# Kernel optimization log

Hardware: AMD Instinct MI355X
Metric: run time of the kernel (lower is better)

## Reference

```python
import jax, jax.numpy as jnp
import numpy as np

N, DF, DR, H, K = 4096, 128, 64, 1024, 10


def _init_linear(key, fan_in, fan_out):
    kw, kb = jax.random.split(key)
    bound = 1.0 / np.sqrt(fan_in)
    W = jax.random.uniform(kw, (fan_in, fan_out), jnp.float32, -bound, bound)
    b = jax.random.uniform(kb, (fan_out,), jnp.float32, -bound, bound)
    return W, b


def setup_inputs() -> dict:
    key = jax.random.key(0)
    ks = jax.random.split(key, 8)
    condition = jax.random.normal(ks[0], (N, DF), jnp.float32)
    tensor = jax.random.normal(ks[1], (N, DR), jnp.float32)
    Win, b_in = _init_linear(ks[2], DF + DR, H)
    W1, b1 = _init_linear(ks[3], H, H)
    W2, b2 = _init_linear(ks[4], H, H)
    W3, b3 = _init_linear(ks[5], H, H)
    Wout, b_out = _init_linear(ks[6], H, DR)
    return {"condition": condition, "tensor": tensor,
            "Win": Win, "b_in": b_in, "W1": W1, "b1": b1,
            "W2": W2, "b2": b2, "W3": W3, "b3": b3,
            "Wout": Wout, "b_out": b_out}


def _mlp(x, Win, b_in, W1, b1, W2, b2, W3, b3, Wout, b_out):
    # FFNN: input layer + 3 hidden layers with Softplus, linear output -> DR
    h = jax.nn.softplus(x @ Win + b_in)
    h = jax.nn.softplus(h @ W1 + b1)
    h = jax.nn.softplus(h @ W2 + b2)
    h = jax.nn.softplus(h @ W3 + b3)
    return h @ Wout + b_out


def reference(condition, tensor, Win, b_in, W1, b1, W2, b2, W3, b3, Wout, b_out):
    # torch.cdist(condition, condition), p=2 -> [N, N]
    sq = jnp.sum(condition * condition, axis=-1)
    d2 = sq[:, None] + sq[None, :] - 2.0 * (condition @ condition.T)
    dist = jnp.sqrt(jnp.maximum(d2, 0.0))
    # torch.topk(dist, 10, dim=1, largest=False) -> k nearest neighbor indices
    _, neighbor_idx = jax.lax.top_k(-dist, K)  # [N, K]
    # gather neighbor groups
    cond_g = condition[neighbor_idx]  # [N, K, DF]
    tens_g = tensor[neighbor_idx]     # [N, K, DR]
    # MongeMapNetwork.pushforward: tensor - MLP(concat(condition, tensor))
    x = jnp.concatenate([cond_g, tens_g], axis=-1)  # [N, K, DF+DR]
    pushed = tens_g - _mlp(x, Win, b_in, W1, b1, W2, b2, W3, b3, Wout, b_out)
    return pushed  # [N, K, DR]
```

## Files before the change

### kernel.cpp

```cpp
#include <hip/hip_runtime.h>
#include <hip/hip_fp16.h>
#include <stdint.h>

typedef unsigned short u16;
typedef unsigned int   u32;
typedef unsigned long long u64;
typedef short v8bf __attribute__((ext_vector_type(8)));
typedef float v4f  __attribute__((ext_vector_type(4)));
typedef u16   v8u  __attribute__((ext_vector_type(8)));

#define NPTS 4096
#define DF   128
#define DR   64
#define HID  1024
#define KNN  10
#define DIN  192
#define NB   512

#define AS1 __attribute__((address_space(1)))
#define AS3 __attribute__((address_space(3)))

__device__ __forceinline__ float bf2f(u16 b){ return __uint_as_float(((unsigned)b)<<16); }
__device__ __forceinline__ u16 f2bf(float f){
  unsigned u = __float_as_uint(f);
  unsigned r = 0x7fffu + ((u>>16)&1u);
  return (u16)((u + r)>>16);
}
__device__ __forceinline__ u16 f2h(float f){
  __half h = __float2half(f);
  return __half_as_ushort(h);
}
__device__ __forceinline__ float softplus_f(float x){
  return x>15.f ? x : __logf(1.f + __expf(x));
}
__device__ __forceinline__ float rdv(const void* p, long j, int fl){
  return fl ? bf2f(((const u16*)p)[j]) : ((const float*)p)[j];
}
__device__ __forceinline__ void gl2lds16(const u16* g, u16* l){
  __builtin_amdgcn_global_load_lds((const AS1 unsigned int*)g, (AS3 unsigned int*)l, 16, 0, 0);
}

constexpr size_t OFF_BAR   = 0;
constexpr size_t OFF_FLAG  = 128;
constexpr size_t OFF_SQ    = 256;
constexpr size_t OFF_NIDX  = OFF_SQ    + 16384;
constexpr size_t OFF_BIAS  = OFF_NIDX  + 163840;
constexpr size_t OFF_CONDF = OFF_BIAS  + 16640;
constexpr size_t OFF_TENSF = OFF_CONDF + 2097152;
constexpr size_t OFF_WTIN  = OFF_TENSF + 1048576;
constexpr size_t OFF_WT1   = OFF_WTIN  + 393216;
constexpr size_t OFF_WT2   = OFF_WT1   + 2097152;
constexpr size_t OFF_WT3   = OFF_WT2   + 2097152;
constexpr size_t OFF_WTO   = OFF_WT3   + 2097152;
constexpr size_t OFF_DIST  = OFF_WTO   + 131072;
constexpr size_t OFF_X     = OFF_DIST  + 33554432;
constexpr size_t OFF_A0    = OFF_X     + 1572864;
constexpr size_t OFF_A1    = OFF_A0    + 8388608;
constexpr size_t OFF_P     = OFF_A1    + 8388608;

__device__ __forceinline__ void gbar(u32* cnt, u32* rel, u32 e){
  __syncthreads();
  if(threadIdx.x == 0){
    __threadfence();
    u32 a = __hip_atomic_fetch_add(cnt, 1u, __ATOMIC_ACQ_REL, __HIP_MEMORY_SCOPE_AGENT);
    if(a == e*NB + (NB-1)){
      __hip_atomic_store(rel, e+1u, __ATOMIC_RELEASE, __HIP_MEMORY_SCOPE_AGENT);
    } else {
      while(__hip_atomic_load(rel, __ATOMIC_ACQUIRE, __HIP_MEMORY_SCOPE_AGENT) <= e)
        __builtin_amdgcn_s_sleep(2);
    }
    __threadfence();
  }
  __syncthreads();
}

__device__ __forceinline__ int detect_fl(const void* cond, u16* SM){
  const u16* c = (const u16*)cond;
  int tid = threadIdx.x, n = 0;
  for(int i=tid; i<8192; i+=256){
    u16 v = c[2*i];
    int e = (v>>7)&0xff;
    n += (e>=96 && e<=158);
  }
  int* cnt = (int*)SM;
  cnt[tid] = n; __syncthreads();
  for(int s=128; s>0; s>>=1){ if(tid<s) cnt[tid]+=cnt[tid+s]; __syncthreads(); }
  int fl = (cnt[0] > 4915) ? 1 : 0;
  __syncthreads();
  return fl;
}

__device__ __forceinline__ void prep_unit(int u, int tid, int fl,
    const void* cond, const void* tens,
    const void* Wi, const void* W1, const void* W2, const void* W3, const void* Wo,
    const void* bi, const void* b1, const void* b2, const void* b3, const void* bo,
    float* condF, float* tensF, float* biasF,
    u16* Oi, u16* O1, u16* O2, u16* O3, u16* Oo,
    float* sq, u16* X, u16* SM){
  if(u < 3089){
    int i = u*256 + tid;
    if(i < 524288){ condF[i] = rdv(cond, i, fl); }
    else if(i < 786432){ tensF[i-524288] = rdv(tens, i-524288, fl); }
    else{
      int j = i - 786432;
      if(j < 1024)      biasF[j] = rdv(bi, j, fl);
      else if(j < 2048) biasF[j] = rdv(b1, j-1024, fl);
      else if(j < 3072) biasF[j] = rdv(b2, j-2048, fl);
      else if(j < 4096) biasF[j] = rdv(b3, j-3072, fl);
      else if(j < 4160) biasF[j] = rdv(bo, j-4096, fl);
    }
  } else if(u < 6417){
    u16 (*tile)[33] = (u16(*)[33])SM;
    int b = u - 3089;
    const void* in; u16* out; int R, C, bx, by;
    if(b < 192)      {              in=Wi; out=Oi; R=192;  C=1024; bx=b&31; by=b>>5; }
    else if(b < 1216){ b -= 192;    in=W1; out=O1; R=1024; C=1024; bx=b&31; by=b>>5; }
    else if(b < 2240){ b -= 1216;   in=W2; out=O2; R=1024; C=1024; bx=b&31; by=b>>5; }
    else if(b < 3264){ b -= 2240;   in=W3; out=O3; R=1024; C=1024; bx=b&31; by=b>>5; }
    else             { b -= 3264;   in=Wo; out=Oo; R=1024; C=64;   bx=b&1;  by=b>>1; }
    int gx = bx*32, gy = by*32;
    int tx = tid&31, ty = tid>>5;
    #pragma unroll
    for(int r=ty; r<32; r+=8){
      size_t idx = (size_t)(gy+r)*C + gx + tx;
      tile[r][tx] = fl ? ((const u16*)in)[idx] : f2bf(((const float*)in)[idx]);
    }
    __syncthreads();
    #pragma unroll
    for(int r=ty; r<32; r+=8) out[(size_t)(gx+r)*R + gy + tx] = tile[tx][r];
  } else if(u < 7441){
    int b = u - 6417;
    int row = b*4 + (tid>>6), lane = tid&63;
    float a = rdv(cond, (long)row*DF + lane, fl);
    float c2 = rdv(cond, (long)row*DF + lane + 64, fl);
    double s = (double)a*a + (double)c2*c2;
    #pragma unroll
    for(int off=32; off>0; off>>=1) s += __shfl_down(s, off, 64);
    if(lane==0) sq[row] = (float)s;
  } else {
    int c = (u-7441)*256 + tid;
    int j = c/48;
    int off = (c - j*48)*4;
    ushort4 o;
    if(off < DF){
      o.x = f2bf(rdv(cond, (long)j*DF + off + 0, fl));
      o.y = f2bf(rdv(cond, (long)j*DF + off + 1, fl));
      o.z = f2bf(rdv(cond, (long)j*DF + off + 2, fl));
      o.w = f2bf(rdv(cond, (long)j*DF + off + 3, fl));
    }else{
      int t2 = off - DF;
      o.x = f2bf(rdv(tens, (long)j*DR + t2 + 0, fl));
      o.y = f2bf(rdv(tens, (long)j*DR + t2 + 1, fl));
      o.z = f2bf(rdv(tens, (long)j*DR + t2 + 2, fl));
      o.w = f2bf(rdv(tens, (long)j*DR + t2 + 3, fl));
    }
    *(ushort4*)&X[(size_t)j*DIN + off] = o;
  }
}

__device__ __forceinline__ void gemm_bt_body(const u16* __restrict__ A,
    const u16* __restrict__ Bt, const float* __restrict__ bias, u16* __restrict__ C,
    int Nc, int Kc, int bid, u16* As, u16* Bs){
  const int xcd = bid&7, slot = bid>>3;
  const int bm = (xcd*4 + (slot>>4)) * 128;
  const int bn = (slot&15) * 64;
  const int tid = threadIdx.x, lane = tid&63, wave = tid>>6;
  const int wm = (wave&1)*64, wn = (wave>>1)*32;
  int c0 = wave*128 + lane, c1 = c0 + 64;
  int r0 = c0>>2, q0 = c0&3, r1 = c1>>2, q1 = c1&3;
  int cb = wave*64 + lane, rb = cb>>2, qb = cb&3;
  const u16* pA0 = A  + (size_t)(bm+r0)*Kc + q0*8;
  const u16* pA1 = A  + (size_t)(bm+r1)*Kc + q1*8;
  const u16* pB  = Bt + (size_t)(bn+rb)*Kc + qb*8;
  u16* lA0 = &As[wave*1024];
  u16* lA1 = &As[wave*1024 + 512];
  u16* lB  = &Bs[wave*512];
  const int m16 = lane&15, q = lane>>4;
  v4f acc[4][2] = {};
  for(int kb=0; kb<Kc; kb+=64){
    gl2lds16(pA0 + kb, lA0);
    gl2lds16(pA1 + kb, lA1);
    gl2lds16(pB  + kb, lB);
    gl2lds16(pA0 + kb + 32, lA0 + 4096);
    gl2lds16(pA1 + kb + 32, lA1 + 4096);
    gl2lds16(pB  + kb + 32, lB + 2048);
    __syncthreads();
    #pragma unroll
    for(int kk=0;kk<2;kk++){
      v8bf a[4], b[2];
      #pragma unroll
      for(int x=0;x<4;x++) a[x] = *(const v8bf*)&As[kk*4096 + (wm + x*16 + m16)*32 + q*8];
      #pragma unroll
      for(int x=0;x<2;x++) b[x] = *(const v8bf*)&Bs[kk*2048 + (wn + x*16 + m16)*32 + q*8];
      #pragma unroll
      for(int mi=0;mi<4;mi++)
        #pragma unroll
        for(int ni=0;ni<2;ni++)
          acc[mi][ni] = __builtin_amdgcn_mfma_f32_16x16x32_bf16(a[mi], b[ni], acc[mi][ni], 0,0,0);
    }
    __syncthreads();
  }
  const int col16 = lane&15, rowq = lane>>4;
  #pragma unroll
  for(int mi=0;mi<4;mi++){
    #pragma unroll
    for(int ni=0;ni<2;ni++){
      int cn = bn + wn + ni*16 + col16;
      float bi = bias[cn];
      #pragma unroll
      for(int r=0;r<4;r++){
        int rw = bm + wm + mi*16 + rowq*4 + r;
        float v = softplus_f(acc[mi][ni][r] + bi);
        C[(size_t)rw*Nc + cn] = f2bf(v);
      }
    }
  }
}

__device__ __forceinline__ void knn_body(const u16* __restrict__ distH,
    const float* __restrict__ condF, int* __restrict__ nidx, int row,
    float* __restrict__ af, int* __restrict__ cand, u64* __restrict__ keys){
  const int lane = threadIdx.x&63;
  af[lane]    = condF[(size_t)row*DF + lane];
  af[lane+64] = condF[(size_t)row*DF + lane + 64];
  const v8u* drow = (const v8u*)(distH + (size_t)row*NPTS);
  v8u vals[8];
  #pragma unroll
  for(int k=0;k<8;k++) vals[k] = drow[lane + k*64];
  u32 mx = 0;
  #pragma unroll
  for(int k=0;k<8;k++)
    #pragma unroll
    for(int e=0;e<8;e++){ u32 v = vals[k][e]; mx = v>mx ? v : mx; }
  #pragma unroll
  for(int off=32; off>0; off>>=1){
    u32 o = (u32)__shfl_down((int)mx, off, 64); mx = o>mx ? o : mx;
  }
  mx = (u32)__shfl((int)mx, 0, 64);
  u32 hi = mx+1, lo = 0;
  for(int it=0; it<17; ++it){
    u32 mid = (lo+hi)>>1;
    int c = 0;
    #pragma unroll
    for(int k=0;k<8;k++)
      #pragma unroll
      for(int e=0;e<8;e++)
        c += (int)__popcll(__ballot((u32)vals[k][e] < mid));
    if(c >= 16){ hi = mid; if(c <= 64) break; }
    else lo = mid;
  }
  const u32 t = hi;
  const u64 below = (1ull<<lane) - 1ull;
  int base = 0;
  #pragma unroll
  for(int k=0;k<8;k++)
    #pragma unroll
    for(int e=0;e<8;e++){
      bool p = (u32)vals[k][e] < t;
      u64 m = __ballot(p);
      if(p){
        int off = base + (int)__popcll(m & below);
        if(off < 64) cand[off] = (lane + k*64)*8 + e;
      }
      base += (int)__popcll(m);
    }
  int cnt = base > 64 ? 64 : base;
  u64 mykey = ~0ULL; int myj = -1;
  if(lane < cnt){
    int j = cand[lane];
    const float4* bp4 = (const float4*)(condF + (size_t)j*DF);
    double s = 0.0;
    #pragma unroll
    for(int v4i=0; v4i<32; v4i++){
      float4 bv = bp4[v4i];
      double d0 = (double)af[v4i*4+0]-(double)bv.x;
      double d1 = (double)af[v4i*4+1]-(double)bv.y;
      double d2 = (double)af[v4i*4+2]-(double)bv.z;
      double d3 = (double)af[v4i*4+3]-(double)bv.w;
      s += d0*d0 + d1*d1 + d2*d2 + d3*d3;
    }
    u64 bits = (u64)__double_as_longlong(s);
    mykey = (bits & ~0xFFFULL) | (u32)j;
    myj = j;
  }
  keys[lane] = mykey;
  if(lane < cnt){
    int rank = 0;
    for(int c2=0;c2<cnt;c2++) rank += (keys[c2] < mykey);
    if(rank < KNN) nidx[row*KNN + rank] = myj;
  }
}

__device__ __forceinline__ void gram_tile(int gb, int fl,
    const u16* __restrict__ condB, const float* __restrict__ condF,
    const float* __restrict__ sq, u16* __restrict__ distH, u16* SM){
  const int bm = (gb&31)*128, bn = (gb>>5)*128;
  const int tid = threadIdx.x, lane = tid&63, wave = tid>>6;
  const int wm = (wave&1)*64, wn = (wave>>1)*64;
  const int m16 = lane&15, q = lane>>4;
  v4f acc[4][4] = {};
  if(fl){
    const int srow = wave*32 + (lane>>2), scol = (lane&3)*8;
    const u16* gA = condB + (size_t)(bm+srow)*DF + scol;
    const u16* gB = condB + (size_t)(bn+srow)*DF + scol;
    u16* lA = &SM[wave*1024];
    u16* lB = &SM[4096 + wave*1024];
    for(int kb=0; kb<DF; kb+=32){
      gl2lds16(gA + kb,                 lA);
      gl2lds16(gA + kb + (size_t)16*DF, lA + 512);
      gl2lds16(gB + kb,                 lB);
      gl2lds16(gB + kb + (size_t)16*DF, lB + 512);
      __syncthreads();
      v8bf a[4], b[4];
      #pragma unroll
      for(int x=0;x<4;x++){
        a[x] = *(const v8bf*)&SM[(wm + x*16 + m16)*32 + q*8];
        b[x] = *(const v8bf*)&SM[4096 + (wn + x*16 + m16)*32 + q*8];
      }
      #pragma unroll
      for(int mi=0;mi<4;mi++)
        #pragma unroll
        for(int ni=0;ni<4;ni++)
          acc[mi][ni] = __builtin_amdgcn_mfma_f32_16x16x32_bf16(a[mi], b[ni], acc[mi][ni], 0,0,0);
      __syncthreads();
    }
  } else {
    u16* Ahi = SM;
    u16* Alo = SM + 5120;
    u16* Bhi = SM + 10240;
    u16* Blo = SM + 15360;
    for(int kb=0; kb<DF; kb+=32){
      #pragma unroll
      for(int t=0;t<4;t++){
        int ch = tid + t*256;
        int r = ch>>3, c = (ch&7)*4;
        float4 av = *(const float4*)&condF[(size_t)(bm+r)*DF + kb + c];
        float4 bv = *(const float4*)&condF[(size_t)(bn+r)*DF + kb + c];
        ushort4 ah, bh, al, bl;
        ah.x=f2bf(av.x); ah.y=f2bf(av.y); ah.z=f2bf(av.z); ah.w=f2bf(av.w);
        bh.x=f2bf(bv.x); bh.y=f2bf(bv.y); bh.z=f2bf(bv.z); bh.w=f2bf(bv.w);
        al.x=f2bf(av.x-bf2f(ah.x)); al.y=f2bf(av.y-bf2f(ah.y));
        al.z=f2bf(av.z-bf2f(ah.z)); al.w=f2bf(av.w-bf2f(ah.w));
        bl.x=f2bf(bv.x-bf2f(bh.x)); bl.y=f2bf(bv.y-bf2f(bh.y));
        bl.z=f2bf(bv.z-bf2f(bh.z)); bl.w=f2bf(bv.w-bf2f(bh.w));
        *(ushort4*)&Ahi[r*40+c] = ah; *(ushort4*)&Bhi[r*40+c] = bh;
        *(ushort4*)&Alo[r*40+c] = al; *(ushort4*)&Blo[r*40+c] = bl;
      }
      __syncthreads();
      v8bf ahf[4], bhf[4], alf[4], blf[4];
      #pragma unroll
      for(int x=0;x<4;x++){
        ahf[x] = *(const v8bf*)&Ahi[(wm + x*16 + m16)*40 + q*8];
        bhf[x] = *(const v8bf*)&Bhi[(wn + x*16 + m16)*40 + q*8];
        alf[x] = *(const v8bf*)&Alo[(wm + x*16 + m16)*40 + q*8];
        blf[x] = *(const v8bf*)&Blo[(wn + x*16 + m16)*40 + q*8];
      }
      #pragma unroll
      for(int mi=0;mi<4;mi++)
        #pragma unroll
        for(int ni=0;ni<4;ni++){
          acc[mi][ni] = __builtin_amdgcn_mfma_f32_16x16x32_bf16(alf[mi], bhf[ni], acc[mi][ni], 0,0,0);
          acc[mi][ni] = __builtin_amdgcn_mfma_f32_16x16x32_bf16(ahf[mi], blf[ni], acc[mi][ni], 0,0,0);
          acc[mi][ni] = __builtin_amdgcn_mfma_f32_16x16x32_bf16(ahf[mi], bhf[ni], acc[mi][ni], 0,0,0);
        }
      __syncthreads();
    }
  }
  const int col16 = lane&15, rowq = lane>>4;
  #pragma unroll
  for(int mi=0;mi<4;mi++){
    #pragma unroll
    for(int ni=0;ni<4;ni++){
      int cj = bn + wn + ni*16 + col16;
      float sqj = sq[cj];
      #pragma unroll
      for(int r=0;r<4;r++){
        int ri = bm + wm + mi*16 + rowq*4 + r;
        float d2 = (sq[ri] + sqj) - 2.0f*acc[mi][ni][r];
        distH[(size_t)ri*NPTS + cj] = f2h(fmaxf(d2, 0.f));
      }
    }
  }
}

__device__ __forceinline__ void gemm_out_body(int obid, const u16* __restrict__ A,
    const u16* __restrict__ Bt, float* __restrict__ Pp, u16* As, u16* Bs){
  const int bm = (obid>>2)*128;
  const int k0 = (obid&3)*256;
  float* P = Pp + (size_t)(obid&3)*262144;
  const int tid = threadIdx.x, lane = tid&63, wave = tid>>6;
  const int wm = wave*32;
  int c0 = wave*128 + lane, c1 = c0 + 64;
  int ra0 = c0>>2, qa0 = c0&3, ra1 = c1>>2, qa1 = c1&3;
  int cb = wave*64 + lane;
  int rb = cb>>2, qb = cb&3;
  const u16* pA0 = A  + (size_t)(bm+ra0)*HID + qa0*8;
  const u16* pA1 = A  + (size_t)(bm+ra1)*HID + qa1*8;
  const u16* pB  = Bt + (size_t)rb*HID + qb*8;
  u16* lA0 = &As[(wave*128     )*8];
  u16* lA1 = &As[(wave*128 + 64)*8];
  u16* lB  = &Bs[(wave*64      )*8];
  const int m16 = lane&15, q = lane>>4;
  v4f acc[2][4] = {};
  for(int kb=k0; kb<k0+256; kb+=32){
    gl2lds16(pA0 + kb, lA0);
    gl2lds16(pA1 + kb, lA1);
    gl2lds16(pB  + kb, lB);
    __syncthreads();
    v8bf a[2], b[4];
    a[0] = *(const v8bf*)&As[(wm + m16)*32 + q*8];
    a[1] = *(const v8bf*)&As[(wm + 16 + m16)*32 + q*8];
    #pragma unroll
    for(int x=0;x<4;x++) b[x] = *(const v8bf*)&Bs[(x*16 + m16)*32 + q*8];
    #pragma unroll
    for(int mi=0;mi<2;mi++)
      #pragma unroll
      for(int ni=0;ni<4;ni++)
        acc[mi][ni] = __builtin_amdgcn_mfma_f32_16x16x32_bf16(a[mi], b[ni], acc[mi][ni], 0,0,0);
    __syncthreads();
  }
  const int col16 = lane&15, rowq = lane>>4;
  #pragma unroll
  for(int mi=0;mi<2;mi++){
    #pragma unroll
    for(int ni=0;ni<4;ni++){
      int cn = ni*16 + col16;
      #pragma unroll
      for(int r=0;r<4;r++){
        int rw = bm + wm + mi*16 + rowq*4 + r;
        P[(size_t)rw*DR + cn] = acc[mi][ni][r];
      }
    }
  }
}

__device__ __forceinline__ void gather_unit(int e, int fl,
    const float* Pp, const float* tensF, const float* biasF,
    const int* nidx, void* outv){
  int m = e>>4;
  int c = (e&15)*4;
  int j = nidx[m] & (NPTS-1);
  size_t rc = (size_t)j*DR + c;
  float4 t  = *(const float4*)&tensF[rc];
  float4 b  = *(const float4*)&biasF[4096 + c];
  float4 p0 = *(const float4*)&Pp[rc];
  float4 p1 = *(const float4*)&Pp[262144 + rc];
  float4 p2 = *(const float4*)&Pp[524288 + rc];
  float4 p3 = *(const float4*)&Pp[786432 + rc];
  float4 v;
  v.x = t.x - (b.x + ((p0.x+p1.x)+(p2.x+p3.x)));
  v.y = t.y - (b.y + ((p0.y+p1.y)+(p2.y+p3.y)));
  v.z = t.z - (b.z + ((p0.z+p1.z)+(p2.z+p3.z)));
  v.w = t.w - (b.w + ((p0.w+p1.w)+(p2.w+p3.w)));
  if(fl){
    ushort4 o; o.x=f2bf(v.x); o.y=f2bf(v.y); o.z=f2bf(v.z); o.w=f2bf(v.w);
    *(ushort4*)&((u16*)outv)[(size_t)m*DR + c] = o;
  }else{
    *(float4*)&((float*)outv)[(size_t)m*DR + c] = v;
  }
}

__global__ void __launch_bounds__(256,2) mega_k(
    const void* cond, const void* tens,
    const void* Wi, const void* W1w, const void* W2w, const void* W3w, const void* Wow,
    const void* bi, const void* b1, const void* b2, const void* b3, const void* bo,
    char* ws, void* outv){
  __shared__ __align__(16) u16 SM[20480];
  const int bid = blockIdx.x, tid = threadIdx.x;

  u32*   bcnt  = (u32*)  (ws + OFF_BAR);
  u32*   brel  = (u32*)  (ws + OFF_BAR + 8);
  float* sqv   = (float*)(ws + OFF_SQ);
  int*   nidx  = (int*)  (ws + OFF_NIDX);
  float* biasF = (float*)(ws + OFF_BIAS);
  float* condF = (float*)(ws + OFF_CONDF);
  float* tensF = (float*)(ws + OFF_TENSF);
  u16*   Wt_in = (u16*)  (ws + OFF_WTIN);
  u16*   Wt1   = (u16*)  (ws + OFF_WT1);
  u16*   Wt2   = (u16*)  (ws + OFF_WT2);
  u16*   Wt3   = (u16*)  (ws + OFF_WT3);
  u16*   Wt_o  = (u16*)  (ws + OFF_WTO);
  u16*   distH = (u16*)  (ws + OFF_DIST);
  u16*   X     = (u16*)  (ws + OFF_X);
  u16*   A0    = (u16*)  (ws + OFF_A0);
  u16*   A1    = (u16*)  (ws + OFF_A1);
  float* Pp    = (float*)(ws + OFF_P);

  const int fl = detect_fl(cond, SM);

  for(int u=bid; u<8209; u+=NB){
    prep_unit(u, tid, fl, cond, tens, Wi, W1w, W2w, W3w, Wow, bi, b1, b2, b3, bo,
              condF, tensF, biasF, Wt_in, Wt1, Wt2, Wt3, Wt_o, sqv, X, SM);
    __syncthreads();
  }
  gbar(bcnt, brel, 0);

  gemm_bt_body(X, Wt_in, biasF, A0, HID, DIN, bid, SM, SM+8192);
  __syncthreads();
  for(int gb=bid; gb<1024; gb+=NB){
    gram_tile(gb, fl, (const u16*)cond, condF, sqv, distH, SM);
    __syncthreads();
  }
  gbar(bcnt, brel, 1);

  const int wv = tid>>6;
  float* kaf  = (float*)SM + wv*128;
  int*   kcan = (int*)((char*)SM + 2048) + wv*64;
  u64*   kkey = (u64*)((char*)SM + 4096) + wv*64;

  if(bid < 256){
    gemm_bt_body(A0, Wt1, biasF+1024, A1, HID, HID, bid,     SM, SM+8192);
    __syncthreads();
    gemm_bt_body(A0, Wt1, biasF+1024, A1, HID, HID, bid+256, SM, SM+8192);
  } else {
    knn_body(distH, condF, nidx, (bid-256)*4 + wv, kaf, kcan, kkey);
  }
  gbar(bcnt, brel, 2);

  if(bid < 256){
    gemm_bt_body(A1, Wt2, biasF+2048, A0, HID, HID, bid,     SM, SM+8192);
    __syncthreads();
    gemm_bt_body(A1, Wt2, biasF+2048, A0, HID, HID, bid+256, SM, SM+8192);
  } else {
    knn_body(distH, condF, nidx, 1024 + (bid-256)*4 + wv, kaf, kcan, kkey);
  }
  gbar(bcnt, brel, 3);

  if(bid < 256){
    gemm_bt_body(A0, Wt3, biasF+3072, A1, HID, HID, bid,     SM, SM+8192);
    __syncthreads();
    gemm_bt_body(A0, Wt3, biasF+3072, A1, HID, HID, bid+256, SM, SM+8192);
  } else {
    knn_body(distH, condF, nidx, 2048 + (bid-256)*4 + wv, kaf, kcan, kkey);
  }
  gbar(bcnt, brel, 4);

  if(bid < 128){
    gemm_out_body(bid, A1, Wt_o, Pp, SM, SM+8192);
  } else if(bid >= 256){
    knn_body(distH, condF, nidx, 3072 + (bid-256)*4 + wv, kaf, kcan, kkey);
  }
  gbar(bcnt, brel, 5);

  for(int u=bid; u<2560; u+=NB)
    gather_unit(u*256 + tid, fl, Pp, tensF, biasF, nidx, outv);
}

__global__ void detect_k(const u16* __restrict__ c, int* __restrict__ flag){
  __shared__ int cnt[256];
  int t = threadIdx.x, n = 0;
  for(int i=t; i<8192; i+=256){
    u16 v = c[2*i];
    int e = (v>>7)&0xff;
    n += (e>=96 && e<=158);
  }
  cnt[t] = n; __syncthreads();
  for(int s=128; s>0; s>>=1){ if(t<s) cnt[t]+=cnt[t+s]; __syncthreads(); }
  if(t==0) *flag = (cnt[0] > 4915) ? 1 : 0;
}

__global__ void prep_k(const void* cond, const void* tens,
    const void* Wi, const void* W1, const void* W2, const void* W3, const void* Wo,
    const void* bi, const void* b1, const void* b2, const void* b3, const void* bo,
    float* condF, float* tensF, float* biasF,
    u16* Oi, u16* O1, u16* O2, u16* O3, u16* Oo,
    float* sq, u16* X, const int* __restrict__ flag){
  __shared__ __align__(16) u16 SM[1056];
  prep_unit(blockIdx.x, threadIdx.x, *flag, cond, tens, Wi, W1, W2, W3, Wo,
            bi, b1, b2, b3, bo, condF, tensF, biasF, Oi, O1, O2, O3, Oo, sq, X, SM);
}

__global__ __launch_bounds__(256,2) void gram_g1_k(const u16* __restrict__ condB,
    const float* __restrict__ condF, const float* __restrict__ sq,
    u16* __restrict__ distH, const int* __restrict__ flag,
    const u16* __restrict__ X, const u16* __restrict__ Wt_in,
    const float* __restrict__ biasF, u16* __restrict__ A0){
  __shared__ __align__(16) u16 SM[20480];
  const int bid = blockIdx.x;
  if(bid < 512){
    gemm_bt_body(X, Wt_in, biasF, A0, HID, DIN, bid, SM, SM+8192);
  } else {
    gram_tile(bid-512, *flag, condB, condF, sq, distH, SM);
  }
}

__global__ __launch_bounds__(256,2) void gemm_knn_k(const u16* __restrict__ A,
    const u16* __restrict__ Bt, const float* __restrict__ bias, u16* __restrict__ C,
    const u16* __restrict__ distH, const float* __restrict__ condF,
    int* __restrict__ nidx, int rowoff){
  __shared__ __align__(16) u16 gsm[12288];
  __shared__ float af[4][DF];
  __shared__ int   cand[4][64];
  __shared__ u64   keys[4][64];
  const int bid = blockIdx.x;
  if(bid < 512){
    gemm_bt_body(A, Bt, bias, C, HID, HID, bid, gsm, gsm+8192);
  } else {
    const int wv = threadIdx.x>>6;
    knn_body(distH, condF, nidx, rowoff + (bid-512)*4 + wv, af[wv], cand[wv], keys[wv]);
  }
}

__global__ __launch_bounds__(256,2) void gemm_bt_k(const u16* __restrict__ A,
    const u16* __restrict__ Bt, const float* __restrict__ bias, u16* __restrict__ C){
  __shared__ __align__(16) u16 As[8192];
  __shared__ __align__(16) u16 Bs[4096];
  gemm_bt_body(A, Bt, bias, C, HID, HID, blockIdx.x, As, Bs);
}

__global__ __launch_bounds__(256,2) void gemm_out_k(const u16* __restrict__ A,
    const u16* __restrict__ Bt, float* __restrict__ Pp){
  __shared__ __align__(16) u16 As[4096];
  __shared__ __align__(16) u16 Bs[2048];
  gemm_out_body(blockIdx.x, A, Bt, Pp, As, Bs);
}

__global__ void gather_k(const float* __restrict__ Pp, const float* __restrict__ tensF,
                         const float* __restrict__ biasF, const int* __restrict__ nidx,
                         void* __restrict__ outv, const int* __restrict__ flag){
  gather_unit(blockIdx.x*256 + threadIdx.x, *flag, Pp, tensF, biasF, nidx, outv);
}

extern "C" void kernel_launch(void* const* d_in, const int* in_sizes, int n_in,
                              void* d_out, int out_size, void* d_ws, size_t ws_size,
                              hipStream_t stream){
  char* ws = (char*)d_ws;
  int*   flag  = (int*)  (ws + OFF_FLAG);
  float* sqv   = (float*)(ws + OFF_SQ);
  int*   nidx  = (int*)  (ws + OFF_NIDX);
  float* biasF = (float*)(ws + OFF_BIAS);
  float* condF = (float*)(ws + OFF_CONDF);
  float* tensF = (float*)(ws + OFF_TENSF);
  u16*   Wt_in = (u16*)  (ws + OFF_WTIN);
  u16*   Wt1   = (u16*)  (ws + OFF_WT1);
  u16*   Wt2   = (u16*)  (ws + OFF_WT2);
  u16*   Wt3   = (u16*)  (ws + OFF_WT3);
  u16*   Wt_o  = (u16*)  (ws + OFF_WTO);
  u16*   distH = (u16*)  (ws + OFF_DIST);
  u16*   X     = (u16*)  (ws + OFF_X);
  u16*   A0    = (u16*)  (ws + OFF_A0);
  u16*   A1    = (u16*)  (ws + OFF_A1);
  float* Pp    = (float*)(ws + OFF_P);

  static int occ_cached = -1;
  if(occ_cached < 0){
    int occ = 0;
    if(hipOccupancyMaxActiveBlocksPerMultiprocessor(&occ, (const void*)mega_k, 256, 0)
       != hipSuccess) occ = 0;
    occ_cached = occ;
  }

  if(occ_cached >= 2){
    hipMemsetAsync(ws + OFF_BAR, 0, 64, stream);
    hipLaunchKernelGGL(mega_k, dim3(NB), dim3(256), 0, stream,
        d_in[0], d_in[1], d_in[2], d_in[4], d_in[6], d_in[8], d_in[10],
        d_in[3], d_in[5], d_in[7], d_in[9], d_in[11], ws, d_out);
    return;
  }

  detect_k <<<1, 256, 0, stream>>>((const u16*)d_in[0], flag);
  prep_k   <<<8209, 256, 0, stream>>>(d_in[0], d_in[1],
                d_in[2], d_in[4], d_in[6], d_in[8], d_in[10],
                d_in[3], d_in[5], d_in[7], d_in[9], d_in[11],
                condF, tensF, biasF, Wt_in, Wt1, Wt2, Wt3, Wt_o, sqv, X, flag);
  gram_g1_k<<<1536, 256, 0, stream>>>((const u16*)d_in[0], condF, sqv, distH, flag,
                                      X, Wt_in, biasF, A0);
  gemm_knn_k<<<1024, 256, 0, stream>>>(A0, Wt1, biasF+1024, A1, distH, condF, nidx, 0);
  gemm_knn_k<<<1024, 256, 0, stream>>>(A1, Wt2, biasF+2048, A0, distH, condF, nidx, 2048);
  gemm_bt_k  <<<512, 256, 0, stream>>>(A0, Wt3, biasF+3072, A1);
  gemm_out_k <<<128, 256, 0, stream>>>(A1, Wt_o, Pp);
  gather_k   <<<2560, 256, 0, stream>>>(Pp, tensF, biasF, nidx, d_out, flag);
}
```

Baseline: 206.6 us.

## Vectorize prep conversion and process two KNN rows per wave to rebalance stages

The prep phase now converts inputs eight elements at a time with vector loads, and the X packing copies bf16 data directly. This cuts the prep unit count. A new knn_body2 handles two rows per wave, so all KNN work now fits in the first two gemm-overlap stages. The third hidden GEMM then runs on all 512 blocks at once, and the output stage no longer carries KNN work. In exchange, each KNN wave holds twice as many registers, which could hurt occupancy.

```diff
diff --git a/kernel.cpp b/kernel.cpp
--- a/kernel.cpp
+++ b/kernel.cpp
@@ -16,6 +16,7 @@
 #define KNN  10
 #define DIN  192
 #define NB   512
+#define PREP_UNITS 5507
 
 #define AS1 __attribute__((address_space(1)))
 #define AS3 __attribute__((address_space(3)))
@@ -90,6 +91,19 @@
   return fl;
 }
 
+__device__ __forceinline__ void cvt8(float* dst, const void* src, long j0, int fl){
+  if(fl){
+    v8u h = *(const v8u*)&((const u16*)src)[j0];
+    float4 a, b;
+    a.x=bf2f(h[0]); a.y=bf2f(h[1]); a.z=bf2f(h[2]); a.w=bf2f(h[3]);
+    b.x=bf2f(h[4]); b.y=bf2f(h[5]); b.z=bf2f(h[6]); b.w=bf2f(h[7]);
+    *(float4*)dst = a; *(float4*)(dst+4) = b;
+  } else {
+    *(float4*)dst     = *(const float4*)&((const float*)src)[j0];
+    *(float4*)(dst+4) = *(const float4*)&((const float*)src)[j0+4];
+  }
+}
+
 __device__ __forceinline__ void prep_unit(int u, int tid, int fl,
     const void* cond, const void* tens,
     const void* Wi, const void* W1, const void* W2, const void* W3, const void* Wo,
@@ -97,21 +111,23 @@
     float* condF, float* tensF, float* biasF,
     u16* Oi, u16* O1, u16* O2, u16* O3, u16* Oo,
     float* sq, u16* X, u16* SM){
-  if(u < 3089){
-    int i = u*256 + tid;
-    if(i < 524288){ condF[i] = rdv(cond, i, fl); }
-    else if(i < 786432){ tensF[i-524288] = rdv(tens, i-524288, fl); }
-    else{
-      int j = i - 786432;
-      if(j < 1024)      biasF[j] = rdv(bi, j, fl);
-      else if(j < 2048) biasF[j] = rdv(b1, j-1024, fl);
-      else if(j < 3072) biasF[j] = rdv(b2, j-2048, fl);
-      else if(j < 4096) biasF[j] = rdv(b3, j-3072, fl);
-      else if(j < 4160) biasF[j] = rdv(bo, j-4096, fl);
-    }
-  } else if(u < 6417){
+  if(u < 387){
+    int v = u*256 + tid;
+    if(v < 65536){ cvt8(condF + (size_t)v*8, cond, (long)v*8, fl); }
+    else if(v < 98304){ int w = v - 65536; cvt8(tensF + (size_t)w*8, tens, (long)w*8, fl); }
+    else if(v < 98824){
+      int j = (v - 98304)*8;
+      const void* src; int off;
+      if(j < 1024){ src=bi; off=j; }
+      else if(j < 2048){ src=b1; off=j-1024; }
+      else if(j < 3072){ src=b2; off=j-2048; }
+      else if(j < 4096){ src=b3; off=j-3072; }
+      else             { src=bo; off=j-4096; }
+      cvt8(biasF + j, src, off, fl);
+    }
+  } else if(u < 3715){
     u16 (*tile)[33] = (u16(*)[33])SM;
-    int b = u - 3089;
+    int b = u - 387;
     const void* in; u16* out; int R, C, bx, by;
     if(b < 192)      {              in=Wi; out=Oi; R=192;  C=1024; bx=b&31; by=b>>5; }
     else if(b < 1216){ b -= 192;    in=W1; out=O1; R=1024; C=1024; bx=b&31; by=b>>5; }
@@ -128,8 +144,8 @@
     __syncthreads();
     #pragma unroll
     for(int r=ty; r<32; r+=8) out[(size_t)(gx+r)*R + gy + tx] = tile[tx][r];
-  } else if(u < 7441){
-    int b = u - 6417;
+  } else if(u < 4739){
+    int b = u - 3715;
     int row = b*4 + (tid>>6), lane = tid&63;
     float a = rdv(cond, (long)row*DF + lane, fl);
     float c2 = rdv(cond, (long)row*DF + lane + 64, fl);
@@ -138,21 +154,24 @@
     for(int off=32; off>0; off>>=1) s += __shfl_down(s, off, 64);
     if(lane==0) sq[row] = (float)s;
   } else {
-    int c = (u-7441)*256 + tid;
+    int c = (u-4739)*256 + tid;
     int j = c/48;
     int off = (c - j*48)*4;
     ushort4 o;
-    if(off < DF){
-      o.x = f2bf(rdv(cond, (long)j*DF + off + 0, fl));
-      o.y = f2bf(rdv(cond, (long)j*DF + off + 1, fl));
-      o.z = f2bf(rdv(cond, (long)j*DF + off + 2, fl));
-      o.w = f2bf(rdv(cond, (long)j*DF + off + 3, fl));
+    if(fl){
+      o = (off < DF) ? *(const ushort4*)&((const u16*)cond)[(size_t)j*DF + off]
+                     : *(const ushort4*)&((const u16*)tens)[(size_t)j*DR + off - DF];
+    } else if(off < DF){
+      o.x = f2bf(((const float*)cond)[(size_t)j*DF + off + 0]);
+      o.y = f2bf(((const float*)cond)[(size_t)j*DF + off + 1]);
+      o.z = f2bf(((const float*)cond)[(size_t)j*DF + off + 2]);
+      o.w = f2bf(((const float*)cond)[(size_t)j*DF + off + 3]);
     }else{
       int t2 = off - DF;
-      o.x = f2bf(rdv(tens, (long)j*DR + t2 + 0, fl));
-      o.y = f2bf(rdv(tens, (long)j*DR + t2 + 1, fl));
-      o.z = f2bf(rdv(tens, (long)j*DR + t2 + 2, fl));
-      o.w = f2bf(rdv(tens, (long)j*DR + t2 + 3, fl));
+      o.x = f2bf(((const float*)tens)[(size_t)j*DR + t2 + 0]);
+      o.y = f2bf(((const float*)tens)[(size_t)j*DR + t2 + 1]);
+      o.z = f2bf(((const float*)tens)[(size_t)j*DR + t2 + 2]);
+      o.w = f2bf(((const float*)tens)[(size_t)j*DR + t2 + 3]);
     }
     *(ushort4*)&X[(size_t)j*DIN + off] = o;
   }
@@ -291,6 +310,116 @@
   }
 }
 
+__device__ __forceinline__ void knn_body2(const u16* __restrict__ distH,
+    const float* __restrict__ condF, int* __restrict__ nidx, int row0, int row1,
+    float* af0, float* af1, int* can0, int* can1, u64* key0, u64* key1){
+  const int lane = threadIdx.x&63;
+  af0[lane]    = condF[(size_t)row0*DF + lane];
+  af0[lane+64] = condF[(size_t)row0*DF + lane + 64];
+  af1[lane]    = condF[(size_t)row1*DF + lane];
+  af1[lane+64] = condF[(size_t)row1*DF + lane + 64];
+  const v8u* dr0 = (const v8u*)(distH + (size_t)row0*NPTS);
+  const v8u* dr1 = (const v8u*)(distH + (size_t)row1*NPTS);
+  v8u v0[8], v1[8];
+  #pragma unroll
+  for(int k=0;k<8;k++){ v0[k] = dr0[lane + k*64]; v1[k] = dr1[lane + k*64]; }
+  u32 m0 = 0, m1 = 0;
+  #pragma unroll
+  for(int k=0;k<8;k++)
+    #pragma unroll
+    for(int e=0;e<8;e++){
+      u32 a = v0[k][e]; m0 = a>m0 ? a : m0;
+      u32 b = v1[k][e]; m1 = b>m1 ? b : m1;
+    }
+  #pragma unroll
+  for(int off=32; off>0; off>>=1){
+    u32 a = (u32)__shfl_down((int)m0, off, 64); m0 = a>m0 ? a : m0;
+    u32 b = (u32)__shfl_down((int)m1, off, 64); m1 = b>m1 ? b : m1;
+  }
+  m0 = (u32)__shfl((int)m0, 0, 64);
+  m1 = (u32)__shfl((int)m1, 0, 64);
+  u32 hi0 = m0+1, lo0 = 0, hi1 = m1+1, lo1 = 0;
+  bool done0 = false, done1 = false;
+  for(int it=0; it<17 && !(done0 && done1); ++it){
+    u32 mid0 = (lo0+hi0)>>1, mid1 = (lo1+hi1)>>1;
+    int c0 = 0, c1 = 0;
+    #pragma unroll
+    for(int k=0;k<8;k++)
+      #pragma unroll
+      for(int e=0;e<8;e++){
+        c0 += ((u32)v0[k][e] < mid0);
+        c1 += ((u32)v1[k][e] < mid1);
+      }
+    #pragma unroll
+    for(int off=32; off>0; off>>=1){
+      c0 += __shfl_down(c0, off, 64);
+      c1 += __shfl_down(c1, off, 64);
+    }
+    c0 = __shfl(c0, 0, 64);
+    c1 = __shfl(c1, 0, 64);
+    if(!done0){ if(c0 >= 16){ hi0 = mid0; if(c0 <= 64) done0 = true; } else lo0 = mid0; }
+    if(!done1){ if(c1 >= 16){ hi1 = mid1; if(c1 <= 64) done1 = true; } else lo1 = mid1; }
+  }
+  const u32 t0 = hi0, t1 = hi1;
+  const u64 below = (1ull<<lane) - 1ull;
+  int base0 = 0, base1 = 0;
+  #pragma unroll
+  for(int k=0;k<8;k++)
+    #pragma unroll
+    for(int e=0;e<8;e++){
+      bool p0 = (u32)v0[k][e] < t0;
+      u64 q0 = __ballot(p0);
+      if(p0){
+        int off = base0 + (int)__popcll(q0 & below);
+        if(off < 64) can0[off] = (lane + k*64)*8 + e;
+      }
+      base0 += (int)__popcll(q0);
+      bool p1 = (u32)v1[k][e] < t1;
+      u64 q1 = __ballot(p1);
+      if(p1){
+        int off = base1 + (int)__popcll(q1 & below);
+        if(off < 64) can1[off] = (lane + k*64)*8 + e;
+      }
+      base1 += (int)__popcll(q1);
+    }
+  int cnt0 = base0 > 64 ? 64 : base0;
+  int cnt1 = base1 > 64 ? 64 : base1;
+  int j0 = (lane < cnt0) ? can0[lane] : 0;
+  int j1 = (lane < cnt1) ? can1[lane] : 0;
+  const float4* p0 = (const float4*)(condF + (size_t)j0*DF);
+  const float4* p1 = (const float4*)(condF + (size_t)j1*DF);
+  double s0 = 0.0, s1 = 0.0;
+  #pragma unroll
+  for(int v4i=0; v4i<32; v4i++){
+    float4 a = p0[v4i], b = p1[v4i];
+    double d0 = (double)af0[v4i*4+0]-(double)a.x;
+    double d1 = (double)af0[v4i*4+1]-(double)a.y;
+    double d2 = (double)af0[v4i*4+2]-(double)a.z;
+    double d3 = (double)af0[v4i*4+3]-(double)a.w;
+    s0 += d0*d0 + d1*d1 + d2*d2 + d3*d3;
+    double e0 = (double)af1[v4i*4+0]-(double)b.x;
+    double e1 = (double)af1[v4i*4+1]-(double)b.y;
+    double e2 = (double)af1[v4i*4+2]-(double)b.z;
+    double e3 = (double)af1[v4i*4+3]-(double)b.w;
+    s1 += e0*e0 + e1*e1 + e2*e2 + e3*e3;
+  }
+  u64 mk0 = ~0ULL, mk1 = ~0ULL;
+  if(lane < cnt0) mk0 = ((u64)__double_as_longlong(s0) & ~0xFFFULL) | (u32)j0;
+  if(lane < cnt1) mk1 = ((u64)__double_as_longlong(s1) & ~0xFFFULL) | (u32)j1;
+  key0[lane] = mk0;
+  key1[lane] = mk1;
+  if(lane < cnt0){
+    int rank = 0;
+    for(int c2=0;c2<cnt0;c2++) rank += (key0[c2] < mk0);
+    if(rank < KNN) nidx[row0*KNN + rank] = j0;
+  }
+  if(lane < cnt1){
+    int rank = 0;
+    for(int c2=0;c2<cnt1;c2++) rank += (key1[c2] < mk1);
+    if(rank < KNN) nidx[row1*KNN + rank] = j1;
+  }
+}
+
 __device__ __forceinline__ void gram_tile(int gb, int fl,
     const u16* __restrict__ condB, const float* __restrict__ condF,
     const float* __restrict__ sq, u16* __restrict__ distH, u16* SM){
@@ -488,7 +617,7 @@
 
   const int fl = detect_fl(cond, SM);
 
-  for(int u=bid; u<8209; u+=NB){
+  for(int u=bid; u<PREP_UNITS; u+=NB){
     prep_unit(u, tid, fl, cond, tens, Wi, W1w, W2w, W3w, Wow, bi, b1, b2, b3, bo,
               condF, tensF, biasF, Wt_in, Wt1, Wt2, Wt3, Wt_o, sqv, X, SM);
     __syncthreads();
@@ -504,16 +633,20 @@
   gbar(bcnt, brel, 1);
 
   const int wv = tid>>6;
-  float* kaf  = (float*)SM + wv*128;
-  int*   kcan = (int*)((char*)SM + 2048) + wv*64;
-  u64*   kkey = (u64*)((char*)SM + 4096) + wv*64;
+  float* kaf0 = (float*)SM + (wv*2+0)*128;
+  float* kaf1 = (float*)SM + (wv*2+1)*128;
+  int*   kc0  = (int*)((char*)SM + 4096) + (wv*2+0)*64;
+  int*   kc1  = (int*)((char*)SM + 4096) + (wv*2+1)*64;
+  u64*   kk0  = (u64*)((char*)SM + 8192) + (wv*2+0)*64;
+  u64*   kk1  = (u64*)((char*)SM + 8192) + (wv*2+1)*64;
 
   if(bid < 256){
     gemm_bt_body(A0, Wt1, biasF+1024, A1, HID, HID, bid,     SM, SM+8192);
     __syncthreads();
     gemm_bt_body(A0, Wt1, biasF+1024, A1, HID, HID, bid+256, SM, SM+8192);
   } else {
-    knn_body(distH, condF, nidx, (bid-256)*4 + wv, kaf, kcan, kkey);
+    int r0 = (bid-256)*4 + wv;
+    knn_body2(distH, condF, nidx, r0, r0 + 1024, kaf0, kaf1, kc0, kc1, kk0, kk1);
   }
   gbar(bcnt, brel, 2);
 
@@ -522,23 +655,16 @@
     __syncthreads();
     gemm_bt_body(A1, Wt2, biasF+2048, A0, HID, HID, bid+256, SM, SM+8192);
   } else {
-    knn_body(distH, condF, nidx, 1024 + (bid-256)*4 + wv, kaf, kcan, kkey);
+    int r0 = 2048 + (bid-256)*4 + wv;
+    knn_body2(distH, condF, nidx, r0, r0 + 1024, kaf0, kaf1, kc0, kc1, kk0, kk1);
   }
   gbar(bcnt, brel, 3);
 
-  if(bid < 256){
-    gemm_bt_body(A0, Wt3, biasF+3072, A1, HID, HID, bid,     SM, SM+8192);
-    __syncthreads();
-    gemm_bt_body(A0, Wt3, biasF+3072, A1, HID, HID, bid+256, SM, SM+8192);
-  } else {
-    knn_body(distH, condF, nidx, 2048 + (bid-256)*4 + wv, kaf, kcan, kkey);
-  }
+  gemm_bt_body(A0, Wt3, biasF+3072, A1, HID, HID, bid, SM, SM+8192);
   gbar(bcnt, brel, 4);
 
   if(bid < 128){
     gemm_out_body(bid, A1, Wt_o, Pp, SM, SM+8192);
-  } else if(bid >= 256){
-    knn_body(distH, condF, nidx, 3072 + (bid-256)*4 + wv, kaf, kcan, kkey);
   }
   gbar(bcnt, brel, 5);
 
@@ -659,7 +785,7 @@
   }
 
   detect_k <<<1, 256, 0, stream>>>((const u16*)d_in[0], flag);
-  prep_k   <<<8209, 256, 0, stream>>>(d_in[0], d_in[1],
+  prep_k   <<<PREP_UNITS, 256, 0, stream>>>(d_in[0], d_in[1],
                 d_in[2], d_in[4], d_in[6], d_in[8], d_in[10],
                 d_in[3], d_in[5], d_in[7], d_in[9], d_in[11],
                 condF, tensF, biasF, Wt_in, Wt1, Wt2, Wt3, Wt_o, sqv, X, flag);
```

Result: no change. 205.7 us (-0.4%).
